# Optimization experiments

Measured on AMD Instinct MI355X. Metric: run time of the kernel, lower is better.

Reference implementation:

```python
import jax, jax.numpy as jnp
import numpy as np

NEG = -1e9  # stands in for -inf in masked_fill; identical softmax output, grad-safe


def _sfu(inputs, fusion, Wr, Wg):
    # SFU: m = [x, f, x*f, x-f]; o = relu(m@Wr)*g + (1-g)*x, g = sigmoid(m@Wg)
    m = jnp.concatenate([inputs, fusion, inputs * fusion, inputs - fusion], axis=-1)
    x = jax.nn.relu(m @ Wr)
    g = jax.nn.sigmoid(m @ Wg)
    return x * g + (1.0 - g) * inputs


def _stage(U, V, cmask, qmask, E, B, p):
    # One Aligner stage = InterAlign followed by SelfAlign. Batch-first layout (b, len, d).
    Wu, bu, Wv, bv, Wri, Wgi, gi, W1, b1, W2, b2, Wrs, Wgs, gs = p
    # ---- InterAlign ----
    Ct = jax.nn.relu(U @ Wu + bu)              # (b, c, d)
    Qt = jax.nn.relu(V @ Wv + bv)              # (b, q, d)
    E0 = jnp.einsum('bcd,bqd->bcq', Ct, Qt)    # (b, c, q)
    if E is not None:
        Es = jax.nn.softmax(jnp.where(cmask[:, :, None] == 0, NEG, E), axis=1)   # softmax over c
        Bs = jax.nn.softmax(jnp.where(cmask[:, None, :] == 0, NEG, B), axis=2)   # softmax over c (cols)
        E = E0 + gi * jnp.einsum('bce,beq->bcq', Bs, Es)
    else:
        E = E0
    Ett = jax.nn.softmax(jnp.where(qmask[:, None, :] == 0, NEG, E), axis=2)
    qctx = jnp.einsum('bcq,bqd->bcd', Ett, V)  # attend question
    h = _sfu(U, qctx, Wri, Wgi)
    # ---- SelfAlign ----
    H1 = jax.nn.relu(h @ W1 + b1)
    H2 = jax.nn.relu(h @ W2 + b2)
    B0 = jnp.einsum('bcd,bed->bce', H1, H2)    # (b, c, c)
    if B is not None:
        B1s = jax.nn.softmax(jnp.where(cmask[:, :, None] == 0, NEG, B), axis=1)
        B2s = jax.nn.softmax(jnp.where(cmask[:, None, :] == 0, NEG, B), axis=2)
        B = B0 + gs * jnp.einsum('bce,bef->bcf', B2s, B1s)
    else:
        B = B0
    c = U.shape[1]
    B = B * (1.0 - jnp.eye(c, dtype=B.dtype))[None]  # masked_fill_(eye, 0.0): zero diagonal
    Btt = jax.nn.softmax(jnp.where(cmask[:, None, :] == 0, NEG, B), axis=2)
    hctx = jnp.einsum('bce,bed->bcd', Btt, h)
    Z = _sfu(h, hctx, Wrs, Wgs)
    return Z, E, B


def setup_inputs() -> dict:
    key = jax.random.key(0)
    b, c_len, q_len, d = 8, 768, 96, 768
    T = 2  # number of aligner stages
    ks = jax.random.split(key, 16)
    s = 0.02
    inp = {
        'U': jax.random.normal(ks[0], (b, c_len, d), jnp.float32),
        'V': jax.random.normal(ks[1], (b, q_len, d), jnp.float32),
        'U_mask': jax.random.randint(ks[2], (b, c_len), 0, 2).astype(jnp.int32),
        'V_mask': jax.random.randint(ks[3], (b, q_len), 0, 2).astype(jnp.int32),
        'Wu': jax.random.normal(ks[4], (T, d, d), jnp.float32) * s,
        'bu': jnp.zeros((T, d), jnp.float32),
        'Wv': jax.random.normal(ks[5], (T, d, d), jnp.float32) * s,
        'bv': jnp.zeros((T, d), jnp.float32),
        'Wr_i': jax.random.normal(ks[6], (T, 4 * d, d), jnp.float32) * s,
        'Wg_i': jax.random.normal(ks[7], (T, 4 * d, d), jnp.float32) * s,
        'gamma_i': jnp.full((T,), 3.0, jnp.float32),
        'W1': jax.random.normal(ks[8], (T, d, d), jnp.float32) * s,
        'b1': jnp.zeros((T, d), jnp.float32),
        'W2': jax.random.normal(ks[9], (T, d, d), jnp.float32) * s,
        'b2': jnp.zeros((T, d), jnp.float32),
        'Wr_s': jax.random.normal(ks[10], (T, 4 * d, d), jnp.float32) * s,
        'Wg_s': jax.random.normal(ks[11], (T, 4 * d, d), jnp.float32) * s,
        'gamma_s': jnp.full((T,), 3.0, jnp.float32),
    }
    return inp


def reference(U, V, U_mask, V_mask, Wu, bu, Wv, bv, Wr_i, Wg_i, gamma_i,
              W1, b1, W2, b2, Wr_s, Wg_s, gamma_s):
    E = None
    B = None
    x = U
    for t in range(Wu.shape[0]):  # fixed small stage loop (align_1 -> align_2)
        p = (Wu[t], bu[t], Wv[t], bv[t], Wr_i[t], Wg_i[t], gamma_i[t],
             W1[t], b1[t], W2[t], b2[t], Wr_s[t], Wg_s[t], gamma_s[t])
        x, E, B = _stage(x, V, U_mask, V_mask, E, B, p)
    return x
```

## Files before the change

kernel.cpp:

```cpp
#include <hip/hip_runtime.h>
#include <math.h>

#define NEGV -1e9f

typedef short bf16x8 __attribute__((ext_vector_type(8)));
typedef float f32x4 __attribute__((ext_vector_type(4)));
typedef unsigned short ushort8v __attribute__((ext_vector_type(8)));

static __device__ __forceinline__ unsigned short f2bf(float f) {
  unsigned int u = __float_as_uint(f);
  unsigned int r = (u + 0x7fffu + ((u >> 16) & 1u)) >> 16;
  return (unsigned short)r;
}
static __device__ __forceinline__ float bf2f(unsigned short u) {
  return __uint_as_float((unsigned int)u << 16);
}

static __device__ __forceinline__ int xcd_swz(int lin, int nwg) {
  int q = nwg >> 3, r = nwg & 7;
  int x = lin & 7, i = lin >> 3;
  return (x < r) ? x * (q + 1) + i : r * (q + 1) + (x - r) * q + i;
}

__device__ __forceinline__ float wred_max(float v) {
  #pragma unroll
  for (int o = 32; o > 0; o >>= 1) v = fmaxf(v, __shfl_down(v, o, 64));
  return v;
}
__device__ __forceinline__ float wred_sum(float v) {
  #pragma unroll
  for (int o = 32; o > 0; o >>= 1) v += __shfl_down(v, o, 64);
  return v;
}

__global__ __launch_bounds__(256)
void softmax_row_mask(const float* __restrict__ X, const int* __restrict__ mask,
                      float* __restrict__ Y, unsigned short* __restrict__ Ybf,
                      int R, int Cn)
{
  int bz = blockIdx.y, r = blockIdx.x, tid = threadIdx.x;
  const float* xr = X + ((size_t)bz * R + r) * Cn;
  const int*   mr = mask + (size_t)bz * Cn;
  float*       yr = Y ? (Y + ((size_t)bz * R + r) * Cn) : nullptr;
  unsigned short* yb = Ybf ? (Ybf + ((size_t)bz * R + r) * Cn) : nullptr;
  __shared__ float sred[4];

  float mx = -INFINITY;
  for (int i = tid; i < Cn; i += 256) {
    float v = (mr[i] != 0) ? xr[i] : NEGV;
    mx = fmaxf(mx, v);
  }
  float wm = wred_max(mx);
  if ((tid & 63) == 0) sred[tid >> 6] = wm;
  __syncthreads();
  mx = fmaxf(fmaxf(sred[0], sred[1]), fmaxf(sred[2], sred[3]));
  __syncthreads();

  float s = 0.f;
  for (int i = tid; i < Cn; i += 256) {
    float v = (mr[i] != 0) ? xr[i] : NEGV;
    s += expf(v - mx);
  }
  float wsv = wred_sum(s);
  if ((tid & 63) == 0) sred[tid >> 6] = wsv;
  __syncthreads();
  s = sred[0] + sred[1] + sred[2] + sred[3];
  float inv = 1.0f / s;

  for (int i = tid; i < Cn; i += 256) {
    float v = (mr[i] != 0) ? xr[i] : NEGV;
    float o = expf(v - mx) * inv;
    if (yr) yr[i] = o;
    if (yb) yb[i] = f2bf(o);
  }
}

__global__ __launch_bounds__(256)
void colsm_stats(const float* __restrict__ X, const int* __restrict__ mask,
                 float* __restrict__ SM, float* __restrict__ SS, int n)
{
  int bz = blockIdx.z;
  const float* Xb = X + (size_t)bz * n * n;
  const int*   mr = mask + (size_t)bz * n;
  __shared__ float T[64][65];
  __shared__ float rm[4][64], rs[4][64];
  int j0 = blockIdx.x * 64, i0 = blockIdx.y * 64;
  int t = threadIdx.x;
  int tr = t >> 4, tc4 = (t & 15) * 4;
  int jj = t & 63, qq = t >> 6;

  #pragma unroll
  for (int r = 0; r < 4; ++r) {
    int i = tr + r * 16;
    float4 v = *reinterpret_cast<const float4*>(Xb + (size_t)(i0 + i) * n + j0 + tc4);
    int mk = mr[i0 + i];
    T[i][tc4 + 0] = mk ? v.x : NEGV;
    T[i][tc4 + 1] = mk ? v.y : NEGV;
    T[i][tc4 + 2] = mk ? v.z : NEGV;
    T[i][tc4 + 3] = mk ? v.w : NEGV;
  }
  __syncthreads();
  float m = -INFINITY, s = 0.f;
  #pragma unroll
  for (int r = 0; r < 16; ++r) {
    float v = T[qq * 16 + r][jj];
    float nm = fmaxf(m, v);
    s = s * expf(m - nm) + expf(v - nm);
    m = nm;
  }
  rm[qq][jj] = m; rs[qq][jj] = s;
  __syncthreads();
  if (t < 64) {
    float m0 = rm[0][t], m1 = rm[1][t], m2 = rm[2][t], m3 = rm[3][t];
    float fm = fmaxf(fmaxf(m0, m1), fmaxf(m2, m3));
    float fs = rs[0][t] * expf(m0 - fm) + rs[1][t] * expf(m1 - fm)
             + rs[2][t] * expf(m2 - fm) + rs[3][t] * expf(m3 - fm);
    size_t base = (((size_t)bz * gridDim.x + blockIdx.x) * gridDim.y + blockIdx.y) * 64 + t;
    SM[base] = fm; SS[base] = fs;
  }
}

__global__ __launch_bounds__(256)
void colsm_emit(const float* __restrict__ X, const int* __restrict__ mask,
                const float* __restrict__ SM, const float* __restrict__ SS,
                unsigned short* __restrict__ Y, int n)
{
  int bz = blockIdx.z;
  const float* Xb = X + (size_t)bz * n * n;
  const int*   mr = mask + (size_t)bz * n;
  unsigned short* Yb = Y + (size_t)bz * n * n;
  __shared__ float T[64][65];
  __shared__ float sm[64], sinv[64];
  int j0 = blockIdx.x * 64, i0 = blockIdx.y * 64;
  int t = threadIdx.x;
  int tr = t >> 4, tc4 = (t & 15) * 4;
  int nt = gridDim.y;

  if (t < 64) {
    size_t base = (((size_t)bz * gridDim.x + blockIdx.x) * nt) * 64 + t;
    float fm = -INFINITY;
    for (int it = 0; it < nt; ++it) fm = fmaxf(fm, SM[base + (size_t)it * 64]);
    float fs = 0.f;
    for (int it = 0; it < nt; ++it)
      fs += SS[base + (size_t)it * 64] * expf(SM[base + (size_t)it * 64] - fm);
    sm[t] = fm; sinv[t] = 1.0f / fs;
  }
  #pragma unroll
  for (int r = 0; r < 4; ++r) {
    int i = tr + r * 16;
    float4 v = *reinterpret_cast<const float4*>(Xb + (size_t)(i0 + i) * n + j0 + tc4);
    int mk = mr[i0 + i];
    T[i][tc4 + 0] = mk ? v.x : NEGV;
    T[i][tc4 + 1] = mk ? v.y : NEGV;
    T[i][tc4 + 2] = mk ? v.z : NEGV;
    T[i][tc4 + 3] = mk ? v.w : NEGV;
  }
  __syncthreads();
  #pragma unroll
  for (int r = 0; r < 4; ++r) {
    int jr = tr + r * 16;
    float fm = sm[jr], inv = sinv[jr];
    ushort4 o;
    o.x = f2bf(expf(T[tc4 + 0][jr] - fm) * inv);
    o.y = f2bf(expf(T[tc4 + 1][jr] - fm) * inv);
    o.z = f2bf(expf(T[tc4 + 2][jr] - fm) * inv);
    o.w = f2bf(expf(T[tc4 + 3][jr] - fm) * inv);
    *reinterpret_cast<ushort4*>(Yb + (size_t)(j0 + jr) * n + i0 + tc4) = o;
  }
}

__global__ __launch_bounds__(256)
void transp_f32(const float* __restrict__ X, float* __restrict__ Y,
                int R, int C, long sX, long sY)
{
  int bz = blockIdx.z;
  X += (size_t)bz * sX;
  Y += (size_t)bz * sY;
  __shared__ float T[64][65];
  int c0 = blockIdx.x * 64, r0 = blockIdx.y * 64;
  int t = threadIdx.x;
  int tr = t >> 4, tc4 = (t & 15) * 4;
  #pragma unroll
  for (int rr = 0; rr < 4; ++rr) {
    int r = tr + rr * 16;
    float4 v = make_float4(0.f, 0.f, 0.f, 0.f);
    if (c0 + tc4 < C)
      v = *reinterpret_cast<const float4*>(X + (size_t)(r0 + r) * C + c0 + tc4);
    T[r][tc4 + 0] = v.x; T[r][tc4 + 1] = v.y;
    T[r][tc4 + 2] = v.z; T[r][tc4 + 3] = v.w;
  }
  __syncthreads();
  #pragma unroll
  for (int rr = 0; rr < 4; ++rr) {
    int cc = tr + rr * 16;
    int gc = c0 + cc;
    if (gc < C) {
      float4 o = make_float4(T[tc4 + 0][cc], T[tc4 + 1][cc], T[tc4 + 2][cc], T[tc4 + 3][cc]);
      *reinterpret_cast<float4*>(Y + (size_t)gc * R + r0 + tc4) = o;
    }
  }
}

__global__ __launch_bounds__(256)
void transp_bf16(const unsigned short* __restrict__ X, unsigned short* __restrict__ Y)
{
  int bz = blockIdx.z;
  X += (size_t)bz * 589824;
  Y += (size_t)bz * 589824;
  __shared__ unsigned short T[64][65];
  int c0 = blockIdx.x * 64, r0 = blockIdx.y * 64;
  int t = threadIdx.x;
  int tr = t >> 4, tc4 = (t & 15) * 4;
  #pragma unroll
  for (int rr = 0; rr < 4; ++rr) {
    int r = tr + rr * 16;
    ushort4 v = *reinterpret_cast<const ushort4*>(X + (size_t)(r0 + r) * 768 + c0 + tc4);
    T[r][tc4 + 0] = v.x; T[r][tc4 + 1] = v.y;
    T[r][tc4 + 2] = v.z; T[r][tc4 + 3] = v.w;
  }
  __syncthreads();
  #pragma unroll
  for (int rr = 0; rr < 4; ++rr) {
    int cc = tr + rr * 16;
    ushort4 o;
    o.x = T[tc4 + 0][cc]; o.y = T[tc4 + 1][cc];
    o.z = T[tc4 + 2][cc]; o.w = T[tc4 + 3][cc];
    *reinterpret_cast<ushort4*>(Y + (size_t)(c0 + cc) * 768 + r0 + tc4) = o;
  }
}

__global__ __launch_bounds__(256)
void transpV(const float* __restrict__ V, unsigned short* __restrict__ VT)
{
  int bz = blockIdx.z;
  const float* Vb = V + (size_t)bz * 96 * 768;
  unsigned short* Yb = VT + (size_t)bz * 768 * 96;
  __shared__ float T[64][65];
  int c0 = blockIdx.x * 64, r0 = blockIdx.y * 64;
  int t = threadIdx.x;
  int tr = t >> 4, tc4 = (t & 15) * 4;
  #pragma unroll
  for (int rr = 0; rr < 4; ++rr) {
    int r = tr + rr * 16;
    int gr = r0 + r;
    float4 v = make_float4(0.f, 0.f, 0.f, 0.f);
    if (gr < 96)
      v = *reinterpret_cast<const float4*>(Vb + (size_t)gr * 768 + c0 + tc4);
    T[r][tc4 + 0] = v.x; T[r][tc4 + 1] = v.y;
    T[r][tc4 + 2] = v.z; T[r][tc4 + 3] = v.w;
  }
  __syncthreads();
  #pragma unroll
  for (int rr = 0; rr < 4; ++rr) {
    int cc = tr + rr * 16;
    int gc = c0 + cc;
    #pragma unroll
    for (int e = 0; e < 4; ++e) {
      int gr = r0 + tc4 + e;
      if (gr < 96) Yb[(size_t)gc * 96 + gr] = f2bf(T[tc4 + e][cc]);
    }
  }
}

__global__ __launch_bounds__(256)
void wprep(const float* __restrict__ S0, const float* __restrict__ S1,
           const float* __restrict__ S2, const float* __restrict__ S3,
           const float* __restrict__ W0, const float* __restrict__ W1a,
           const float* __restrict__ W2a, const float* __restrict__ W3a,
           unsigned short* __restrict__ Wt, unsigned short* __restrict__ WuT)
{
  int z = blockIdx.z;
  __shared__ float T[64][65];
  int n0 = blockIdx.x * 64;
  int t = threadIdx.x;
  int tr = t >> 4, tc4 = (t & 15) * 4;

  if (blockIdx.y < 36) {
    const float* W = (z == 0) ? S0 : (z == 1) ? S1 : (z == 2) ? S2 : S3;
    unsigned short* Y = Wt + (size_t)z * 768 * 2304;
    int k0 = blockIdx.y * 64;
    #pragma unroll
    for (int r = 0; r < 4; ++r) {
      int k = tr + r * 16;
      int gk = k0 + k;
      float4 v = *reinterpret_cast<const float4*>(W + (size_t)gk * 768 + n0 + tc4);
      if (gk < 768) {
        float4 u = *reinterpret_cast<const float4*>(W + (size_t)(gk + 2304) * 768 + n0 + tc4);
        v.x += u.x; v.y += u.y; v.z += u.z; v.w += u.w;
      } else if (gk < 1536) {
        float4 u = *reinterpret_cast<const float4*>(W + (size_t)(gk + 1536) * 768 + n0 + tc4);
        v.x -= u.x; v.y -= u.y; v.z -= u.z; v.w -= u.w;
      }
      T[k][tc4 + 0] = v.x; T[k][tc4 + 1] = v.y; T[k][tc4 + 2] = v.z; T[k][tc4 + 3] = v.w;
    }
    __syncthreads();
    #pragma unroll
    for (int r = 0; r < 4; ++r) {
      int n = tr + r * 16;
      ushort4 o;
      o.x = f2bf(T[tc4 + 0][n]); o.y = f2bf(T[tc4 + 1][n]);
      o.z = f2bf(T[tc4 + 2][n]); o.w = f2bf(T[tc4 + 3][n]);
      *reinterpret_cast<ushort4*>(Y + (size_t)(n0 + n) * 2304 + k0 + tc4) = o;
    }
  } else {
    const float* W = (z == 0) ? W0 : (z == 1) ? W1a : (z == 2) ? W2a : W3a;
    unsigned short* Y = WuT + (size_t)z * 768 * 768;
    int k0 = (blockIdx.y - 36) * 64;
    #pragma unroll
    for (int r = 0; r < 4; ++r) {
      int k = tr + r * 16;
      float4 v = *reinterpret_cast<const float4*>(W + (size_t)(k0 + k) * 768 + n0 + tc4);
      T[k][tc4 + 0] = v.x; T[k][tc4 + 1] = v.y; T[k][tc4 + 2] = v.z; T[k][tc4 + 3] = v.w;
    }
    __syncthreads();
    #pragma unroll
    for (int r = 0; r < 4; ++r) {
      int n = tr + r * 16;
      ushort4 o;
      o.x = f2bf(T[tc4 + 0][n]); o.y = f2bf(T[tc4 + 1][n]);
      o.z = f2bf(T[tc4 + 2][n]); o.w = f2bf(T[tc4 + 3][n]);
      *reinterpret_cast<ushort4*>(Y + (size_t)(n0 + n) * 768 + k0 + tc4) = o;
    }
  }
}

__global__ __launch_bounds__(256)
void cast_bf16(const float* __restrict__ X, unsigned short* __restrict__ Y, int n8)
{
  int idx = blockIdx.x * 256 + threadIdx.x;
  if (idx >= n8) return;
  float4 a0 = *reinterpret_cast<const float4*>(X + (size_t)idx * 8);
  float4 a1 = *reinterpret_cast<const float4*>(X + (size_t)idx * 8 + 4);
  ushort8v o;
  o[0] = f2bf(a0.x); o[1] = f2bf(a0.y); o[2] = f2bf(a0.z); o[3] = f2bf(a0.w);
  o[4] = f2bf(a1.x); o[5] = f2bf(a1.y); o[6] = f2bf(a1.z); o[7] = f2bf(a1.w);
  *reinterpret_cast<ushort8v*>(Y + (size_t)idx * 8) = o;
}


template<int NB, int WAVES>
__global__ __launch_bounds__(64 * WAVES)
void mfma_gemm(const unsigned short* __restrict__ A,
               const unsigned short* __restrict__ Bt0,
               const unsigned short* __restrict__ Bt1,
               const float* __restrict__ bias0, const float* __restrict__ bias1,
               const float* __restrict__ alphap, const float* __restrict__ C0,
               float* __restrict__ F0, float* __restrict__ F1,
               unsigned short* __restrict__ O0, unsigned short* __restrict__ O1,
               int M, int N, int K,
               long sA, long sB, long sC0, long sC,
               int relu, int zerodiag,
               const unsigned short* __restrict__ Xc, unsigned short* __restrict__ McO)
{
  const int RG = WAVES / 4;
  const int TM = RG * 48;
  __shared__ unsigned short As[2][TM * 32];
  __shared__ unsigned short Bs0[2][2048];
  __shared__ unsigned short Bs1[2][NB == 2 ? 2048 : 16];

  int nx = gridDim.x, ny = gridDim.y;
  int nwg = nx * ny * gridDim.z;
  int lin = blockIdx.x + nx * (blockIdx.y + ny * blockIdx.z);
  int sw = xcd_swz(lin, nwg);
  int bxi = sw % nx; int rest = sw / nx;
  int byi = rest % ny; int bz = rest / ny;

  A   += (size_t)bz * sA;
  Bt0 += (size_t)bz * sB;
  if (NB == 2) Bt1 += (size_t)bz * sB;
  const float* C0b = C0 ? (C0 + (size_t)bz * sC0) : nullptr;

  int tid = threadIdx.x;
  int w = tid >> 6, l = tid & 63;
  int m0 = byi * TM, n0 = bxi * 64;
  int wr = w >> 2, wc = w & 3;

  int g8 = (((l & 3) ^ ((l >> 3) & 3))) * 8;
  int rowA = w * 16 + (l >> 2); if (rowA > TM - 1) rowA = TM - 1;
  int rB = n0 + (w & 3) * 16 + (l >> 2); if (rB > N - 1) rB = N - 1;
  const unsigned short* srcA  = A + (size_t)(m0 + rowA) * K + g8;
  const unsigned short* srcB0 = Bt0 + (size_t)rB * K + g8;
  const unsigned short* srcB1 = (NB == 2) ? Bt1 + (size_t)rB * K + g8 : nullptr;

#define GG_STAGE(kt, bi) do { int kk0 = (kt) * 32;                                                                        \
    if (w < TM / 16)                                                                                                      \
      __builtin_amdgcn_global_load_lds((const unsigned int*)(srcA + kk0),  (unsigned int*)&As[bi][0]  + w * 256, 16, 0, 0); \
    if (w < 4)                                                                                                            \
      __builtin_amdgcn_global_load_lds((const unsigned int*)(srcB0 + kk0), (unsigned int*)&Bs0[bi][0] + w * 256, 16, 0, 0); \
    if (NB == 2 && w >= 4)                                                                                                \
      __builtin_amdgcn_global_load_lds((const unsigned int*)(srcB1 + kk0), (unsigned int*)&Bs1[bi][0] + (w - 4) * 256, 16, 0, 0); \
  } while (0)

  f32x4 a0[3] = {};
  f32x4 a1v[3] = {};

  const int NT = K / 32;
  int prm = ((l >> 4) ^ ((l >> 1) & 3)) * 8;
  GG_STAGE(0, 0);
  __syncthreads();
  int cur = 0;
  for (int kt = 0; kt < NT; ++kt) {
    if (kt + 1 < NT) GG_STAGE(kt + 1, cur ^ 1);

    bf16x8 af[3];
    #pragma unroll
    for (int i = 0; i < 3; ++i) {
      int off = (wr * 48 + i * 16 + (l & 15)) * 32 + prm;
      af[i] = *reinterpret_cast<const bf16x8*>(&As[cur][off]);
    }
    int offB = (wc * 16 + (l & 15)) * 32 + prm;
    bf16x8 b0 = *reinterpret_cast<const bf16x8*>(&Bs0[cur][offB]);
    #pragma unroll
    for (int i = 0; i < 3; ++i)
      a0[i] = __builtin_amdgcn_mfma_f32_16x16x32_bf16(af[i], b0, a0[i], 0, 0, 0);
    if (NB == 2) {
      bf16x8 b1 = *reinterpret_cast<const bf16x8*>(&Bs1[cur][offB]);
      #pragma unroll
      for (int i = 0; i < 3; ++i)
        a1v[i] = __builtin_amdgcn_mfma_f32_16x16x32_bf16(af[i], b1, a1v[i], 0, 0, 0);
    }
    __syncthreads();
    cur ^= 1;
  }
#undef GG_STAGE

  float alpha = alphap ? alphap[0] : 1.0f;
  float* F0b = F0 ? F0 + (size_t)bz * sC : nullptr;
  float* F1b = F1 ? F1 + (size_t)bz * sC : nullptr;
  unsigned short* O0b = O0 ? O0 + (size_t)bz * sC : nullptr;
  unsigned short* O1b = O1 ? O1 + (size_t)bz * sC : nullptr;
  const unsigned short* Xcb = Xc ? Xc + (size_t)bz * 589824 : nullptr;
  unsigned short* Mcb = McO ? McO + (size_t)bz * 1179648 : nullptr;

  #pragma unroll
  for (int i = 0; i < 3; ++i) {
    #pragma unroll
    for (int qq = 0; qq < 4; ++qq) {
      int gm = m0 + wr * 48 + i * 16 + (l >> 4) * 4 + qq;
      int gn = n0 + wc * 16 + (l & 15);
      if (gn >= N) continue;
      size_t oidx = (size_t)gm * N + gn;
      float v = alpha * a0[i][qq];
      if (bias0) v += bias0[gn];
      if (relu) v = fmaxf(v, 0.f);
      if (C0b) v += C0b[oidx];
      if (zerodiag && gm == gn) v = 0.f;
      if (Mcb) {
        float xv = bf2f(Xcb[(size_t)gm * 768 + gn]);
        size_t mrow = (size_t)gm * 1536 + gn;
        Mcb[mrow]        = f2bf(v);
        Mcb[mrow + 768]  = f2bf(xv * v);
      }
      if (F0b) F0b[oidx] = v;
      if (O0b) O0b[oidx] = f2bf(v);
      if (NB == 2) {
        float v1 = alpha * a1v[i][qq];
        if (bias1) v1 += bias1[gn];
        if (relu) v1 = fmaxf(v1, 0.f);
        if (F1b) F1b[oidx] = v1;
        if (O1b) O1b[oidx] = f2bf(v1);
      }
    }
  }
}

__global__ __launch_bounds__(512)
void mfma_relu_pair(const unsigned short* __restrict__ A1g,
                    const unsigned short* __restrict__ B1g,
                    const float* __restrict__ bias1g, unsigned short* __restrict__ O1g,
                    const unsigned short* __restrict__ A2g,
                    const unsigned short* __restrict__ B2g,
                    const float* __restrict__ bias2g, unsigned short* __restrict__ O2g)
{
  const int K = 768, N = 768, NT = 24;
  __shared__ unsigned short As[2][3072];
  __shared__ unsigned short Bs0[2][2048];

  int nx = gridDim.x, ny = gridDim.y;
  int nwg = nx * ny;
  int lin = blockIdx.x + nx * blockIdx.y;
  int sw = xcd_swz(lin, nwg);
  int bxi = sw % nx; int byi = sw / nx;

  const unsigned short* A; const unsigned short* Bt;
  const float* bias; unsigned short* O;
  int m0;
  if (byi < 64) { A = A1g; Bt = B1g; bias = bias1g; O = O1g; m0 = byi * 96; }
  else          { A = A2g; Bt = B2g; bias = bias2g; O = O2g; m0 = (byi - 64) * 96; }

// ... 386 lines not shown
      __builtin_amdgcn_global_load_lds((const unsigned int*)(srcG + kk0), (unsigned int*)&Bgs[bi][0] + (w - 4) * 256, 16, 0, 0); \
  } while (0)

  f32x4 aR[3] = {};
  f32x4 aG[3] = {};

  int prm = ((l >> 4) ^ ((l >> 1) & 3)) * 8;
  SFU_STAGE(0, 0);
  __syncthreads();
  int cur = 0;
  for (int kt = 0; kt < NT; ++kt) {
    if (kt + 1 < NT) SFU_STAGE(kt + 1, cur ^ 1);

    bf16x8 af[3];
    #pragma unroll
    for (int i = 0; i < 3; ++i) {
      int off = (wr * 48 + i * 16 + (l & 15)) * 32 + prm;
      af[i] = *reinterpret_cast<const bf16x8*>(&As[cur][off]);
    }
    int offB = (wc * 16 + (l & 15)) * 32 + prm;
    bf16x8 br = *reinterpret_cast<const bf16x8*>(&Brs[cur][offB]);
    bf16x8 bg = *reinterpret_cast<const bf16x8*>(&Bgs[cur][offB]);
    #pragma unroll
    for (int i = 0; i < 3; ++i) {
      aR[i] = __builtin_amdgcn_mfma_f32_16x16x32_bf16(af[i], br, aR[i], 0, 0, 0);
      aG[i] = __builtin_amdgcn_mfma_f32_16x16x32_bf16(af[i], bg, aG[i], 0, 0, 0);
    }
    __syncthreads();
    cur ^= 1;
  }
#undef SFU_STAGE

  #pragma unroll
  for (int i = 0; i < 3; ++i) {
    #pragma unroll
    for (int qq = 0; qq < 4; ++qq) {
      int gm = m0 + wr * 48 + i * 16 + (l >> 4) * 4 + qq;
      int gn = n0 + wc * 16 + (l & 15);
      float r = fmaxf(aR[i][qq], 0.f);
      float g = 1.0f / (1.0f + expf(-aG[i][qq]));
      float xv = Xres[(size_t)gm * 768 + gn];
      float z = r * g + (1.0f - g) * xv;
      Z[(size_t)gm * 768 + gn] = z;
      if (Zb) Zb[(size_t)gm * 768 + gn] = f2bf(z);
    }
  }
}

static void launch_mfma1(const unsigned short* A, const unsigned short* Bt,
                         const float* bias, const float* alphap, const float* C0,
                         float* F0, unsigned short* O0,
                         int M, int N, int K, long sA, long sB, long sC0, long sC,
                         int relu, int zd, int batch, int tm, hipStream_t s,
                         const unsigned short* xcat = nullptr, unsigned short* mco = nullptr)
{
  dim3 g((N + 63) / 64, M / tm, batch);
  if (tm == 48)
    mfma_gemm<1, 4><<<g, 256, 0, s>>>(A, Bt, nullptr, bias, nullptr, alphap, C0,
                                      F0, nullptr, O0, nullptr, M, N, K, sA, sB, sC0, sC, relu, zd,
                                      xcat, mco);
  else
    mfma_gemm<1, 8><<<g, 512, 0, s>>>(A, Bt, nullptr, bias, nullptr, alphap, C0,
                                      F0, nullptr, O0, nullptr, M, N, K, sA, sB, sC0, sC, relu, zd,
                                      xcat, mco);
}

static void launch_mfma2(const unsigned short* A, const unsigned short* Bt0,
                         const unsigned short* Bt1, const float* bias0, const float* bias1,
                         unsigned short* O0, unsigned short* O1,
                         int M, int N, int K, long sA, long sB,
                         int relu, int batch, hipStream_t s)
{
  dim3 g((N + 63) / 64, M / 96, batch);
  mfma_gemm<2, 8><<<g, 512, 0, s>>>(A, Bt0, Bt1, bias0, bias1, nullptr, nullptr,
                                    nullptr, nullptr, O0, O1, M, N, K, sA, sB, 0, sA,
                                    relu, 0, nullptr, nullptr);
}

extern "C" void kernel_launch(void* const* d_in, const int* in_sizes, int n_in,
                              void* d_out, int out_size, void* d_ws, size_t ws_size,
                              hipStream_t stream)
{
  const int b = 8, c = 768, q = 96, d = 768, T = 2;
  const float* U   = (const float*)d_in[0];
  const float* V   = (const float*)d_in[1];
  const int*   Um  = (const int*)d_in[2];
  const int*   Vm  = (const int*)d_in[3];
  const float* Wu  = (const float*)d_in[4];
  const float* bu  = (const float*)d_in[5];
  const float* Wv  = (const float*)d_in[6];
  const float* bv  = (const float*)d_in[7];
  const float* Wri = (const float*)d_in[8];
  const float* Wgi = (const float*)d_in[9];
  const float* gi  = (const float*)d_in[10];
  const float* W1  = (const float*)d_in[11];
  const float* b1  = (const float*)d_in[12];
  const float* W2  = (const float*)d_in[13];
  const float* b2  = (const float*)d_in[14];
  const float* Wrs = (const float*)d_in[15];
  const float* Wgs = (const float*)d_in[16];
  const float* gs  = (const float*)d_in[17];
  float* out = (float*)d_out;

  const size_t big = (size_t)b * c * d;
  const size_t smE = (size_t)b * c * q;
  float* ws   = (float*)d_ws;
  float* xbuf = ws + 0 * big;
  float* h    = ws + 1 * big;
  float* Bm   = ws + 2 * big;
  float* t1   = ws + 3 * big;
  float* t2   = ws + 4 * big;
  float* t3   = ws + 5 * big;
  float* t4   = ws + 6 * big;
  float* Ebuf = ws + 7 * big;
  float* E0b  = Ebuf + smE;
  float* Esb  = E0b + smE;
  float* spare = Esb + smE;
  float* slotE = spare + smE;
  float* WTf  = slotE + big / 2;

  unsigned short* Mc2 = (unsigned short*)t1;
  unsigned short* Wt  = (unsigned short*)t4;
  unsigned short* t1h = (unsigned short*)t1;
  unsigned short* XB0 = (unsigned short*)t3;
  unsigned short* XB1 = (unsigned short*)t2;
  unsigned short* t3h2 = XB0 + big;
  unsigned short* slotEb = (unsigned short*)slotE;
  unsigned short* H1b = t1h;
  unsigned short* H2b = H1b + big;
  float* SMst = spare;
  float* SSst = spare + 73728;
  unsigned short* WuT = (unsigned short*)WTf;
  unsigned short* WvT  = WuT  + (size_t)d * d;
  unsigned short* W1T  = WvT  + (size_t)d * d;
  unsigned short* W2T  = W1T  + (size_t)d * d;
  unsigned short* Vb16 = W2T  + (size_t)d * d;
  unsigned short* Qtbb = Vb16 + smE;
  unsigned short* VTb  = Qtbb + smE;
  unsigned short* EsTb = VTb  + smE;

  const long cd = (long)c * d, cq = (long)c * q, qd = (long)q * d, cc = (long)c * c;
  const size_t dd = (size_t)d * d;
  const size_t wslice = (size_t)768 * 2304;
  const int cast_big = (int)(big / 8);
  (void)ws_size; (void)E0b;

  const float* x = U;
  for (int t = 0; t < T; ++t) {
    const float* Writ = Wri + (size_t)t * 4 * dd;
    const float* Wgit = Wgi + (size_t)t * 4 * dd;
    const float* Wrst = Wrs + (size_t)t * 4 * dd;
    const float* Wgst = Wgs + (size_t)t * 4 * dd;

    wprep<<<dim3(12, 48, 4), 256, 0, stream>>>(Writ, Wgit, Wrst, Wgst,
                                               Wu + t * dd, Wv + t * dd,
                                               W1 + t * dd, W2 + t * dd, Wt, WuT);
    if (t == 0) {
      cast_bf16<<<dim3((int)(smE / 8 / 256)), 256, 0, stream>>>(V, Vb16, (int)(smE / 8));
      transpV<<<dim3(12, 2, b), 256, 0, stream>>>(V, VTb);
      cast_bf16<<<dim3(cast_big / 256), 256, 0, stream>>>(x, XB0, cast_big);
    }

    mfma_relu_pair<<<dim3(12, 72), 512, 0, stream>>>(XB0, WuT, bu + t * d, t1h,
                                                     Vb16, WvT, bv + t * d, Qtbb);
    if (t == 0) {
      launch_mfma1(t1h, Qtbb, nullptr, nullptr, nullptr, Ebuf, nullptr,
                   c, q, d, cd, qd, 0, cq, 0, 0, b, 48, stream);
    } else {
      transp_f32<<<dim3(2, 12, b), 256, 0, stream>>>(Ebuf, Esb, c, q, cq, cq);
      softmax_row_mask<<<dim3(q, b), 256, 0, stream>>>(Esb, Um, nullptr, EsTb, q, c);
      mfma_dualE<<<dim3(2, 16, b), 256, 0, stream>>>(t1h, Qtbb, t3h2, EsTb,
                                                     gi + t, Ebuf,
                                                     c, q, d, c, cd, qd, cc, cq, cq);
    }
    qctx_fused<<<dim3(12, 8, b), 512, 0, stream>>>(Ebuf, Vm, VTb, XB0, Mc2);
    sfu_mfma<<<dim3(12, 64), 512, 0, stream>>>(Mc2, XB0, Wt, Wt + wslice, x, h, XB1);
    launch_mfma2(XB1, W1T, W2T, b1 + t * d, b2 + t * d, H1b, H2b,
                 b * c, d, d, 0, 0, 1, 1, stream);
    if (t == 0) {
      launch_mfma1(H1b, H2b, nullptr, nullptr, nullptr, Bm, nullptr,
                   c, c, d, cd, cd, 0, cc, 0, 1, b, 96, stream);
    } else {
      colsm_stats<<<dim3(12, 12, b), 256, 0, stream>>>(Bm, Um, SMst, SSst, c);
      colsm_emit<<<dim3(12, 12, b), 256, 0, stream>>>(Bm, Um, SMst, SSst, slotEb, c);
      mfma_dual2<<<dim3(12, 8, b), 512, 0, stream>>>(H1b, H2b, t3h2, slotEb,
                                                     gs + t, Bm,
                                                     c, c, d, cd, cd, cc, cc, cc, 1);
    }
    softmax_row_mask<<<dim3(c, b), 256, 0, stream>>>(Bm, Um, nullptr, t3h2, c, c);
    transp_bf16<<<dim3(12, 12, b), 256, 0, stream>>>(XB1, slotEb);
    launch_mfma1(t3h2, slotEb, nullptr, nullptr, nullptr, nullptr, nullptr,
                 c, d, c, cc, cd, 0, cd, 0, 0, b, 96, stream, XB1, Mc2);
    float* zdst = (t == T - 1) ? out : xbuf;
    unsigned short* zb16 = (t == T - 1) ? nullptr : XB0;
    sfu_mfma<<<dim3(12, 64), 512, 0, stream>>>(Mc2, XB1, Wt + 2 * wslice, Wt + 3 * wslice,
                                               h, zdst, zb16);

    x = xbuf;
  }
}
```

Baseline: 633.0 us.

## Merge small softmax, transpose and weight-prep kernels into combined multi-role launches

Two block-indexed multi-role kernels replace several small launches. `fused_tail` runs the row softmax of B, the bf16 transpose of h, and the column-softmax statistics for the next stage in one grid. `fused_prep` runs the weight transposition together with the column-softmax emit that the next stage's dual GEMM needs. This moves the column statistics from the start of the next stage to the end of the current one and removes launch gaps and serialization between independent small kernels. The cost is hard-coded sizes (768, 12 tiles) and more complex buffer-lifetime ordering through `slotEb` and `SMst`.

Result: faster. 619.9 us (-2.1%).

```diff
diff --git a/kernel.cpp b/kernel.cpp
--- a/kernel.cpp
+++ b/kernel.cpp
@@ -72,100 +72,6 @@
     float o = expf(v - mx) * inv;
     if (yr) yr[i] = o;
     if (yb) yb[i] = f2bf(o);
-  }
-}
-
-__global__ __launch_bounds__(256)
-void colsm_stats(const float* __restrict__ X, const int* __restrict__ mask,
-                 float* __restrict__ SM, float* __restrict__ SS, int n)
-{
-  int bz = blockIdx.z;
-  const float* Xb = X + (size_t)bz * n * n;
-  const int*   mr = mask + (size_t)bz * n;
-  __shared__ float T[64][65];
-  __shared__ float rm[4][64], rs[4][64];
-  int j0 = blockIdx.x * 64, i0 = blockIdx.y * 64;
-  int t = threadIdx.x;
-  int tr = t >> 4, tc4 = (t & 15) * 4;
-  int jj = t & 63, qq = t >> 6;
-
-  #pragma unroll
-  for (int r = 0; r < 4; ++r) {
-    int i = tr + r * 16;
-    float4 v = *reinterpret_cast<const float4*>(Xb + (size_t)(i0 + i) * n + j0 + tc4);
-    int mk = mr[i0 + i];
-    T[i][tc4 + 0] = mk ? v.x : NEGV;
-    T[i][tc4 + 1] = mk ? v.y : NEGV;
-    T[i][tc4 + 2] = mk ? v.z : NEGV;
-    T[i][tc4 + 3] = mk ? v.w : NEGV;
-  }
-  __syncthreads();
-  float m = -INFINITY, s = 0.f;
-  #pragma unroll
-  for (int r = 0; r < 16; ++r) {
-    float v = T[qq * 16 + r][jj];
-    float nm = fmaxf(m, v);
-    s = s * expf(m - nm) + expf(v - nm);
-    m = nm;
-  }
-  rm[qq][jj] = m; rs[qq][jj] = s;
-  __syncthreads();
-  if (t < 64) {
-    float m0 = rm[0][t], m1 = rm[1][t], m2 = rm[2][t], m3 = rm[3][t];
-    float fm = fmaxf(fmaxf(m0, m1), fmaxf(m2, m3));
-    float fs = rs[0][t] * expf(m0 - fm) + rs[1][t] * expf(m1 - fm)
-             + rs[2][t] * expf(m2 - fm) + rs[3][t] * expf(m3 - fm);
-    size_t base = (((size_t)bz * gridDim.x + blockIdx.x) * gridDim.y + blockIdx.y) * 64 + t;
-    SM[base] = fm; SS[base] = fs;
-  }
-}
-
-__global__ __launch_bounds__(256)
-void colsm_emit(const float* __restrict__ X, const int* __restrict__ mask,
-                const float* __restrict__ SM, const float* __restrict__ SS,
-                unsigned short* __restrict__ Y, int n)
-{
-  int bz = blockIdx.z;
-  const float* Xb = X + (size_t)bz * n * n;
-  const int*   mr = mask + (size_t)bz * n;
-  unsigned short* Yb = Y + (size_t)bz * n * n;
-  __shared__ float T[64][65];
-  __shared__ float sm[64], sinv[64];
-  int j0 = blockIdx.x * 64, i0 = blockIdx.y * 64;
-  int t = threadIdx.x;
-  int tr = t >> 4, tc4 = (t & 15) * 4;
-  int nt = gridDim.y;
-
-  if (t < 64) {
-    size_t base = (((size_t)bz * gridDim.x + blockIdx.x) * nt) * 64 + t;
-    float fm = -INFINITY;
-    for (int it = 0; it < nt; ++it) fm = fmaxf(fm, SM[base + (size_t)it * 64]);
-    float fs = 0.f;
-    for (int it = 0; it < nt; ++it)
-      fs += SS[base + (size_t)it * 64] * expf(SM[base + (size_t)it * 64] - fm);
-    sm[t] = fm; sinv[t] = 1.0f / fs;
-  }
-  #pragma unroll
-  for (int r = 0; r < 4; ++r) {
-    int i = tr + r * 16;
-    float4 v = *reinterpret_cast<const float4*>(Xb + (size_t)(i0 + i) * n + j0 + tc4);
-    int mk = mr[i0 + i];
-    T[i][tc4 + 0] = mk ? v.x : NEGV;
-    T[i][tc4 + 1] = mk ? v.y : NEGV;
-    T[i][tc4 + 2] = mk ? v.z : NEGV;
-    T[i][tc4 + 3] = mk ? v.w : NEGV;
-  }
-  __syncthreads();
-  #pragma unroll
-  for (int r = 0; r < 4; ++r) {
-    int jr = tr + r * 16;
-    float fm = sm[jr], inv = sinv[jr];
-    ushort4 o;
-    o.x = f2bf(expf(T[tc4 + 0][jr] - fm) * inv);
-    o.y = f2bf(expf(T[tc4 + 1][jr] - fm) * inv);
-    o.z = f2bf(expf(T[tc4 + 2][jr] - fm) * inv);
-    o.w = f2bf(expf(T[tc4 + 3][jr] - fm) * inv);
-    *reinterpret_cast<ushort4*>(Yb + (size_t)(j0 + jr) * n + i0 + tc4) = o;
   }
 }
 
@@ -198,34 +104,6 @@
       float4 o = make_float4(T[tc4 + 0][cc], T[tc4 + 1][cc], T[tc4 + 2][cc], T[tc4 + 3][cc]);
       *reinterpret_cast<float4*>(Y + (size_t)gc * R + r0 + tc4) = o;
     }
-  }
-}
-
-__global__ __launch_bounds__(256)
-void transp_bf16(const unsigned short* __restrict__ X, unsigned short* __restrict__ Y)
-{
-  int bz = blockIdx.z;
-  X += (size_t)bz * 589824;
-  Y += (size_t)bz * 589824;
-  __shared__ unsigned short T[64][65];
-  int c0 = blockIdx.x * 64, r0 = blockIdx.y * 64;
-  int t = threadIdx.x;
-  int tr = t >> 4, tc4 = (t & 15) * 4;
-  #pragma unroll
-  for (int rr = 0; rr < 4; ++rr) {
-    int r = tr + rr * 16;
-    ushort4 v = *reinterpret_cast<const ushort4*>(X + (size_t)(r0 + r) * 768 + c0 + tc4);
-    T[r][tc4 + 0] = v.x; T[r][tc4 + 1] = v.y;
-    T[r][tc4 + 2] = v.z; T[r][tc4 + 3] = v.w;
-  }
-  __syncthreads();
-  #pragma unroll
-  for (int rr = 0; rr < 4; ++rr) {
-    int cc = tr + rr * 16;
-    ushort4 o;
-    o.x = T[tc4 + 0][cc]; o.y = T[tc4 + 1][cc];
-    o.z = T[tc4 + 2][cc]; o.w = T[tc4 + 3][cc];
-    *reinterpret_cast<ushort4*>(Y + (size_t)(c0 + cc) * 768 + r0 + tc4) = o;
   }
 }
 
@@ -263,68 +141,6 @@
 }
 
 __global__ __launch_bounds__(256)
-void wprep(const float* __restrict__ S0, const float* __restrict__ S1,
-           const float* __restrict__ S2, const float* __restrict__ S3,
-           const float* __restrict__ W0, const float* __restrict__ W1a,
-           const float* __restrict__ W2a, const float* __restrict__ W3a,
-           unsigned short* __restrict__ Wt, unsigned short* __restrict__ WuT)
-{
-  int z = blockIdx.z;
-  __shared__ float T[64][65];
-  int n0 = blockIdx.x * 64;
-  int t = threadIdx.x;
-  int tr = t >> 4, tc4 = (t & 15) * 4;
-
-  if (blockIdx.y < 36) {
-    const float* W = (z == 0) ? S0 : (z == 1) ? S1 : (z == 2) ? S2 : S3;
-    unsigned short* Y = Wt + (size_t)z * 768 * 2304;
-    int k0 = blockIdx.y * 64;
-    #pragma unroll
-    for (int r = 0; r < 4; ++r) {
-      int k = tr + r * 16;
-      int gk = k0 + k;
-      float4 v = *reinterpret_cast<const float4*>(W + (size_t)gk * 768 + n0 + tc4);
-      if (gk < 768) {
-        float4 u = *reinterpret_cast<const float4*>(W + (size_t)(gk + 2304) * 768 + n0 + tc4);
-        v.x += u.x; v.y += u.y; v.z += u.z; v.w += u.w;
-      } else if (gk < 1536) {
-        float4 u = *reinterpret_cast<const float4*>(W + (size_t)(gk + 1536) * 768 + n0 + tc4);
-        v.x -= u.x; v.y -= u.y; v.z -= u.z; v.w -= u.w;
-      }
-      T[k][tc4 + 0] = v.x; T[k][tc4 + 1] = v.y; T[k][tc4 + 2] = v.z; T[k][tc4 + 3] = v.w;
-    }
-    __syncthreads();
-    #pragma unroll
-    for (int r = 0; r < 4; ++r) {
-      int n = tr + r * 16;
-      ushort4 o;
-      o.x = f2bf(T[tc4 + 0][n]); o.y = f2bf(T[tc4 + 1][n]);
-      o.z = f2bf(T[tc4 + 2][n]); o.w = f2bf(T[tc4 + 3][n]);
-      *reinterpret_cast<ushort4*>(Y + (size_t)(n0 + n) * 2304 + k0 + tc4) = o;
-    }
-  } else {
-    const float* W = (z == 0) ? W0 : (z == 1) ? W1a : (z == 2) ? W2a : W3a;
-    unsigned short* Y = WuT + (size_t)z * 768 * 768;
-    int k0 = (blockIdx.y - 36) * 64;
-    #pragma unroll
-    for (int r = 0; r < 4; ++r) {
-      int k = tr + r * 16;
-      float4 v = *reinterpret_cast<const float4*>(W + (size_t)(k0 + k) * 768 + n0 + tc4);
-      T[k][tc4 + 0] = v.x; T[k][tc4 + 1] = v.y; T[k][tc4 + 2] = v.z; T[k][tc4 + 3] = v.w;
-    }
-    __syncthreads();
-    #pragma unroll
-    for (int r = 0; r < 4; ++r) {
-      int n = tr + r * 16;
-      ushort4 o;
-      o.x = f2bf(T[tc4 + 0][n]); o.y = f2bf(T[tc4 + 1][n]);
-      o.z = f2bf(T[tc4 + 2][n]); o.w = f2bf(T[tc4 + 3][n]);
-      *reinterpret_cast<ushort4*>(Y + (size_t)(n0 + n) * 768 + k0 + tc4) = o;
-    }
-  }
-}
-
-__global__ __launch_bounds__(256)
 void cast_bf16(const float* __restrict__ X, unsigned short* __restrict__ Y, int n8)
 {
   int idx = blockIdx.x * 256 + threadIdx.x;
@@ -335,6 +151,228 @@
   o[0] = f2bf(a0.x); o[1] = f2bf(a0.y); o[2] = f2bf(a0.z); o[3] = f2bf(a0.w);
   o[4] = f2bf(a1.x); o[5] = f2bf(a1.y); o[6] = f2bf(a1.z); o[7] = f2bf(a1.w);
   *reinterpret_cast<ushort8v*>(Y + (size_t)idx * 8) = o;
+}
+
+__global__ __launch_bounds__(256)
+void fused_tail(const float* __restrict__ Bm, const int* __restrict__ Um,
+                unsigned short* __restrict__ Btt,
+                const unsigned short* __restrict__ Hb, unsigned short* __restrict__ HT,
+                float* __restrict__ SM, float* __restrict__ SS)
+{
+  int bid = blockIdx.x;
+  int tid = threadIdx.x;
+
+  if (bid < 6144) {
+    int bz = bid / 768, r = bid - bz * 768;
+    const float* xr = Bm + ((size_t)bz * 768 + r) * 768;
+    const int*   mr = Um + (size_t)bz * 768;
+    unsigned short* yb = Btt + ((size_t)bz * 768 + r) * 768;
+    __shared__ float sred[4];
+
+    float mx = -INFINITY;
+    for (int i = tid; i < 768; i += 256) {
+      float v = (mr[i] != 0) ? xr[i] : NEGV;
+      mx = fmaxf(mx, v);
+    }
+    float wm = wred_max(mx);
+    if ((tid & 63) == 0) sred[tid >> 6] = wm;
+    __syncthreads();
+    mx = fmaxf(fmaxf(sred[0], sred[1]), fmaxf(sred[2], sred[3]));
+    __syncthreads();
+    float s = 0.f;
+    for (int i = tid; i < 768; i += 256) {
+      float v = (mr[i] != 0) ? xr[i] : NEGV;
+      s += expf(v - mx);
+    }
+    float wsv = wred_sum(s);
+    if ((tid & 63) == 0) sred[tid >> 6] = wsv;
+    __syncthreads();
+    s = sred[0] + sred[1] + sred[2] + sred[3];
+    float inv = 1.0f / s;
+    for (int i = tid; i < 768; i += 256) {
+      float v = (mr[i] != 0) ? xr[i] : NEGV;
+      yb[i] = f2bf(expf(v - mx) * inv);
+    }
+  } else if (bid < 7296) {
+    int idx = bid - 6144;
+    int bx = idx % 12; idx /= 12;
+    int by = idx % 12; int bz = idx / 12;
+    const unsigned short* X = Hb + (size_t)bz * 589824;
+    unsigned short* Y = HT + (size_t)bz * 589824;
+    __shared__ unsigned short T[64][65];
+    int c0 = bx * 64, r0 = by * 64;
+    int tr = tid >> 4, tc4 = (tid & 15) * 4;
+    #pragma unroll
+    for (int rr = 0; rr < 4; ++rr) {
+      int r = tr + rr * 16;
+      ushort4 v = *reinterpret_cast<const ushort4*>(X + (size_t)(r0 + r) * 768 + c0 + tc4);
+      T[r][tc4 + 0] = v.x; T[r][tc4 + 1] = v.y;
+      T[r][tc4 + 2] = v.z; T[r][tc4 + 3] = v.w;
+    }
+    __syncthreads();
+    #pragma unroll
+    for (int rr = 0; rr < 4; ++rr) {
+      int cc = tr + rr * 16;
+      ushort4 o;
+      o.x = T[tc4 + 0][cc]; o.y = T[tc4 + 1][cc];
+      o.z = T[tc4 + 2][cc]; o.w = T[tc4 + 3][cc];
+      *reinterpret_cast<ushort4*>(Y + (size_t)(c0 + cc) * 768 + r0 + tc4) = o;
+    }
+  } else {
+    int idx = bid - 7296;
+    int bx = idx % 12; idx /= 12;
+    int by = idx % 12; int bz = idx / 12;
+    const float* Xb = Bm + (size_t)bz * 589824;
+    const int*   mr = Um + (size_t)bz * 768;
+    __shared__ float T[64][65];
+    __shared__ float rm[4][64], rs[4][64];
+    int j0 = bx * 64, i0 = by * 64;
+    int tr = tid >> 4, tc4 = (tid & 15) * 4;
+    int jj = tid & 63, qq = tid >> 6;
+
+    #pragma unroll
+    for (int r = 0; r < 4; ++r) {
+      int i = tr + r * 16;
+      float4 v = *reinterpret_cast<const float4*>(Xb + (size_t)(i0 + i) * 768 + j0 + tc4);
+      int mk = mr[i0 + i];
+      T[i][tc4 + 0] = mk ? v.x : NEGV;
+      T[i][tc4 + 1] = mk ? v.y : NEGV;
+      T[i][tc4 + 2] = mk ? v.z : NEGV;
+      T[i][tc4 + 3] = mk ? v.w : NEGV;
+    }
+    __syncthreads();
+    float m = -INFINITY, s = 0.f;
+    #pragma unroll
+    for (int r = 0; r < 16; ++r) {
+      float v = T[qq * 16 + r][jj];
+      float nm = fmaxf(m, v);
+      s = s * expf(m - nm) + expf(v - nm);
+      m = nm;
+    }
+    rm[qq][jj] = m; rs[qq][jj] = s;
+    __syncthreads();
+    if (tid < 64) {
+      float m0 = rm[0][tid], m1 = rm[1][tid], m2 = rm[2][tid], m3 = rm[3][tid];
+      float fm = fmaxf(fmaxf(m0, m1), fmaxf(m2, m3));
+      float fs = rs[0][tid] * expf(m0 - fm) + rs[1][tid] * expf(m1 - fm)
+               + rs[2][tid] * expf(m2 - fm) + rs[3][tid] * expf(m3 - fm);
+      size_t base = (((size_t)bz * 12 + bx) * 12 + by) * 64 + tid;
+      SM[base] = fm; SS[base] = fs;
+    }
+  }
+}
+
+__global__ __launch_bounds__(256)
+void fused_prep(const float* __restrict__ S0, const float* __restrict__ S1,
+                const float* __restrict__ S2, const float* __restrict__ S3,
+                const float* __restrict__ W0, const float* __restrict__ W1a,
+                const float* __restrict__ W2a, const float* __restrict__ W3a,
+                unsigned short* __restrict__ Wt, unsigned short* __restrict__ WuT,
+                const float* __restrict__ Bm, const int* __restrict__ Um,
+                const float* __restrict__ SM, const float* __restrict__ SS,
+                unsigned short* __restrict__ B1sT)
+{
+  int bid = blockIdx.x;
+  int tid = threadIdx.x;
+  int tr = tid >> 4, tc4 = (tid & 15) * 4;
+
+  if (bid < 2304) {
+    int z = bid / 576;
+    int rem = bid - z * 576;
+    int by = rem / 12, bx = rem - by * 12;
+    __shared__ float T[64][65];
+    int n0 = bx * 64;
+
+    if (by < 36) {
+      const float* W = (z == 0) ? S0 : (z == 1) ? S1 : (z == 2) ? S2 : S3;
+      unsigned short* Y = Wt + (size_t)z * 768 * 2304;
+      int k0 = by * 64;
+      #pragma unroll
+      for (int r = 0; r < 4; ++r) {
+        int k = tr + r * 16;
+        int gk = k0 + k;
+        float4 v = *reinterpret_cast<const float4*>(W + (size_t)gk * 768 + n0 + tc4);
+        if (gk < 768) {
+          float4 u = *reinterpret_cast<const float4*>(W + (size_t)(gk + 2304) * 768 + n0 + tc4);
+          v.x += u.x; v.y += u.y; v.z += u.z; v.w += u.w;
+        } else if (gk < 1536) {
+          float4 u = *reinterpret_cast<const float4*>(W + (size_t)(gk + 1536) * 768 + n0 + tc4);
+          v.x -= u.x; v.y -= u.y; v.z -= u.z; v.w -= u.w;
+        }
+        T[k][tc4 + 0] = v.x; T[k][tc4 + 1] = v.y; T[k][tc4 + 2] = v.z; T[k][tc4 + 3] = v.w;
+      }
+      __syncthreads();
+      #pragma unroll
+      for (int r = 0; r < 4; ++r) {
+        int n = tr + r * 16;
+        ushort4 o;
+        o.x = f2bf(T[tc4 + 0][n]); o.y = f2bf(T[tc4 + 1][n]);
+        o.z = f2bf(T[tc4 + 2][n]); o.w = f2bf(T[tc4 + 3][n]);
+        *reinterpret_cast<ushort4*>(Y + (size_t)(n0 + n) * 2304 + k0 + tc4) = o;
+      }
+    } else {
+      const float* W = (z == 0) ? W0 : (z == 1) ? W1a : (z == 2) ? W2a : W3a;
+      unsigned short* Y = WuT + (size_t)z * 768 * 768;
+      int k0 = (by - 36) * 64;
+      #pragma unroll
+      for (int r = 0; r < 4; ++r) {
+        int k = tr + r * 16;
+        float4 v = *reinterpret_cast<const float4*>(W + (size_t)(k0 + k) * 768 + n0 + tc4);
+        T[k][tc4 + 0] = v.x; T[k][tc4 + 1] = v.y; T[k][tc4 + 2] = v.z; T[k][tc4 + 3] = v.w;
+      }
+      __syncthreads();
+      #pragma unroll
+      for (int r = 0; r < 4; ++r) {
+        int n = tr + r * 16;
+        ushort4 o;
+        o.x = f2bf(T[tc4 + 0][n]); o.y = f2bf(T[tc4 + 1][n]);
+        o.z = f2bf(T[tc4 + 2][n]); o.w = f2bf(T[tc4 + 3][n]);
+        *reinterpret_cast<ushort4*>(Y + (size_t)(n0 + n) * 768 + k0 + tc4) = o;
+      }
+    }
+  } else {
+    int idx = bid - 2304;
+    int bx = idx % 12; idx /= 12;
+    int by = idx % 12; int bz = idx / 12;
+    const float* Xb = Bm + (size_t)bz * 589824;
+    const int*   mr = Um + (size_t)bz * 768;
+    unsigned short* Yb = B1sT + (size_t)bz * 589824;
+    __shared__ float T2[64][65];
+    __shared__ float sm[64], sinv[64];
+    int j0 = bx * 64, i0 = by * 64;
+
+    if (tid < 64) {
+      size_t base = (((size_t)bz * 12 + bx) * 12) * 64 + tid;
+      float fm = -INFINITY;
+      for (int it = 0; it < 12; ++it) fm = fmaxf(fm, SM[base + (size_t)it * 64]);
+      float fs = 0.f;
+      for (int it = 0; it < 12; ++it)
+        fs += SS[base + (size_t)it * 64] * expf(SM[base + (size_t)it * 64] - fm);
+      sm[tid] = fm; sinv[tid] = 1.0f / fs;
+    }
+    #pragma unroll
+    for (int r = 0; r < 4; ++r) {
+      int i = tr + r * 16;
+      float4 v = *reinterpret_cast<const float4*>(Xb + (size_t)(i0 + i) * 768 + j0 + tc4);
+      int mk = mr[i0 + i];
+      T2[i][tc4 + 0] = mk ? v.x : NEGV;
+      T2[i][tc4 + 1] = mk ? v.y : NEGV;
+      T2[i][tc4 + 2] = mk ? v.z : NEGV;
+      T2[i][tc4 + 3] = mk ? v.w : NEGV;
+    }
+    __syncthreads();
+    #pragma unroll
+    for (int r = 0; r < 4; ++r) {
+      int jr = tr + r * 16;
+      float fm = sm[jr], inv = sinv[jr];
+      ushort4 o;
+      o.x = f2bf(expf(T2[tc4 + 0][jr] - fm) * inv);
+      o.y = f2bf(expf(T2[tc4 + 1][jr] - fm) * inv);
+      o.z = f2bf(expf(T2[tc4 + 2][jr] - fm) * inv);
+      o.w = f2bf(expf(T2[tc4 + 3][jr] - fm) * inv);
+      *reinterpret_cast<ushort4*>(Yb + (size_t)(j0 + jr) * 768 + i0 + tc4) = o;
+    }
+  }
 }
 
 
@@ -1027,9 +1065,11 @@
     const float* Wrst = Wrs + (size_t)t * 4 * dd;
     const float* Wgst = Wgs + (size_t)t * 4 * dd;
 
-    wprep<<<dim3(12, 48, 4), 256, 0, stream>>>(Writ, Wgit, Wrst, Wgst,
-                                               Wu + t * dd, Wv + t * dd,
-                                               W1 + t * dd, W2 + t * dd, Wt, WuT);
+    int prep_blocks = (t == 0) ? 2304 : (2304 + 1152);
+    fused_prep<<<dim3(prep_blocks), 256, 0, stream>>>(
+        Writ, Wgit, Wrst, Wgst,
+        Wu + t * dd, Wv + t * dd, W1 + t * dd, W2 + t * dd, Wt, WuT,
+        Bm, Um, SMst, SSst, slotEb);
     if (t == 0) {
       cast_bf16<<<dim3((int)(smE / 8 / 256)), 256, 0, stream>>>(V, Vb16, (int)(smE / 8));
       transpV<<<dim3(12, 2, b), 256, 0, stream>>>(V, VTb);
@@ -1056,14 +1096,13 @@
       launch_mfma1(H1b, H2b, nullptr, nullptr, nullptr, Bm, nullptr,
                    c, c, d, cd, cd, 0, cc, 0, 1, b, 96, stream);
     } else {
-      colsm_stats<<<dim3(12, 12, b), 256, 0, stream>>>(Bm, Um, SMst, SSst, c);
-      colsm_emit<<<dim3(12, 12, b), 256, 0, stream>>>(Bm, Um, SMst, SSst, slotEb, c);
       mfma_dual2<<<dim3(12, 8, b), 512, 0, stream>>>(H1b, H2b, t3h2, slotEb,
                                                      gs + t, Bm,
                                                      c, c, d, cd, cd, cc, cc, cc, 1);
     }
-    softmax_row_mask<<<dim3(c, b), 256, 0, stream>>>(Bm, Um, nullptr, t3h2, c, c);
-    transp_bf16<<<dim3(12, 12, b), 256, 0, stream>>>(XB1, slotEb);
+    int tail_blocks = 6144 + 1152 + ((t < T - 1) ? 1152 : 0);
+    fused_tail<<<dim3(tail_blocks), 256, 0, stream>>>(Bm, Um, t3h2, XB1, slotEb,
+                                                      SMst, SSst);
     launch_mfma1(t3h2, slotEb, nullptr, nullptr, nullptr, nullptr, nullptr,
                  c, d, c, cc, cd, 0, cd, 0, 0, b, 96, stream, XB1, Mc2);
     float* zdst = (t == T - 1) ? out : xbuf;
```
